# Performance work log

Measured on AMD Instinct MI355X. Metric: run time of the kernel, lower is better.

The kernel has to match this reference:

```python
import jax, jax.numpy as jnp
import numpy as np

D_MODEL = 512
N_HEADS = 8
D_FF = 2048

def _linear_params(key, d_in, d_out):
    kw, kb = jax.random.split(key)
    bound = 1.0 / np.sqrt(d_in)
    W = jax.random.uniform(kw, (d_in, d_out), minval=-bound, maxval=bound, dtype=jnp.float32)
    b = jax.random.uniform(kb, (d_out,), minval=-bound, maxval=bound, dtype=jnp.float32)
    return W, b

def setup_inputs() -> dict:
    key = jax.random.key(0)
    ks = jax.random.split(key, 7)
    x = jax.random.normal(ks[0], (4, 2048, D_MODEL), dtype=jnp.float32)
    Wq, bq = _linear_params(ks[1], D_MODEL, D_MODEL)
    Wk, bk = _linear_params(ks[2], D_MODEL, D_MODEL)
    Wv, bv = _linear_params(ks[3], D_MODEL, D_MODEL)
    W1, b1 = _linear_params(ks[4], D_MODEL, D_FF)
    W2, b2 = _linear_params(ks[5], D_FF, D_MODEL)
    g1 = jnp.ones((D_MODEL,), jnp.float32); be1 = jnp.zeros((D_MODEL,), jnp.float32)
    g2 = jnp.ones((D_MODEL,), jnp.float32); be2 = jnp.zeros((D_MODEL,), jnp.float32)
    return {"x": x, "Wq": Wq, "bq": bq, "Wk": Wk, "bk": bk, "Wv": Wv, "bv": bv,
            "W1": W1, "b1": b1, "W2": W2, "b2": b2,
            "g1": g1, "be1": be1, "g2": g2, "be2": be2}

def _layernorm(x, g, b, eps=1e-5):
    mu = jnp.mean(x, axis=-1, keepdims=True)
    var = jnp.mean(jnp.square(x - mu), axis=-1, keepdims=True)
    return (x - mu) * jax.lax.rsqrt(var + eps) * g + b

def reference(x, Wq, bq, Wk, bk, Wv, bv, W1, b1, W2, b2, g1, be1, g2, be2):
    B, S, D = x.shape
    H = N_HEADS
    Dh = D // H
    residual = x
    xn = _layernorm(x, g1, be1)
    # [B,S,D] -> [B,H,S,Dh]
    q = (xn @ Wq + bq).reshape(B, S, H, Dh).transpose(0, 2, 1, 3)
    k = (xn @ Wk + bk).reshape(B, S, H, Dh).transpose(0, 2, 1, 3)
    v = (xn @ Wv + bv).reshape(B, S, H, Dh).transpose(0, 2, 1, 3)
    # sigmoid pointwise attention, scaled by sqrt(d_model) (not head dim)
    scores = jnp.einsum('bhsd,bhtd->bhst', q, k) / jnp.sqrt(jnp.float32(D))
    attn = jax.nn.sigmoid(scores)
    out = jnp.einsum('bhst,bhtd->bhsd', attn, v)
    out = out.transpose(0, 2, 1, 3).reshape(B, S, D)
    x = residual + out  # dropout=0 (eval)
    residual = x
    xn = _layernorm(x, g2, be2)
    ffn = jax.nn.relu(xn @ W1 + b1) @ W2 + b2
    return residual + ffn
```

## Files before the change

### kernel.cpp

```cpp
#include <hip/hip_runtime.h>
#include <hip/hip_bf16.h>
#include <math.h>

#define D_MODEL 512
#define N_HEADS 8
#define D_HEAD 64
#define D_FF 2048
#define SEQ 2048
#define BATCH 4
#define NTOK (BATCH * SEQ)
#define QSCALE 0.04419417382415922f
#define QSCALE_L2E (-QSCALE * 1.44269504089f)

typedef unsigned short ushort_t;
typedef __attribute__((ext_vector_type(8))) short short8;
typedef __attribute__((ext_vector_type(4))) float float4v;

static __device__ __forceinline__ ushort_t f2bf(float f) {
    union { float f; unsigned int i; } c; c.f = f;
    unsigned int i = c.i;
    unsigned int r = (i + 0x7FFFu + ((i >> 16) & 1u)) >> 16;
    return (ushort_t)r;
}

static __device__ __forceinline__ unsigned int pack2bf(float a, float b) {
    union { __hip_bfloat162 h; unsigned int u; } c;
    c.h = __float22bfloat162_rn(make_float2(a, b));
    return c.u;
}

static __device__ __forceinline__ float sig2(float x) {
    return __builtin_amdgcn_rcpf(1.0f + __builtin_amdgcn_exp2f(x));
}

__global__ __launch_bounds__(256) void k_prep_weights(const float* __restrict__ Wq,
                                                      const float* __restrict__ Wk,
                                                      const float* __restrict__ Wv,
                                                      const float* __restrict__ W1,
                                                      const float* __restrict__ W2,
                                                      ushort_t* __restrict__ Wqkvt,
                                                      ushort_t* __restrict__ W1t,
                                                      ushort_t* __restrict__ W2t) {
    int id = blockIdx.x * 256 + threadIdx.x;
    if (id < 3 * 262144) {
        int m = id >> 18, r = id & 262143;
        int k = r >> 9, n = r & 511;
        const float* src = (m == 0) ? Wq : ((m == 1) ? Wk : Wv);
        Wqkvt[((size_t)m * 512 + n) * 512 + k] = f2bf(src[r]);
        return;
    }
    int id2 = id - 3 * 262144;
    if (id2 < 1048576) {
        int k = id2 >> 11, n = id2 & 2047;
        W1t[(size_t)n * 512 + k] = f2bf(W1[id2]);
        return;
    }
    int id3 = id2 - 1048576;
    if (id3 < 1048576) {
        int k = id3 >> 9, n = id3 & 511;
        W2t[(size_t)n * 2048 + k] = f2bf(W2[id3]);
    }
}

__global__ __launch_bounds__(256) void k_layernorm(const float* __restrict__ X,
                                                   const float* __restrict__ g,
                                                   const float* __restrict__ be,
                                                   ushort_t* __restrict__ Out) {
    int row  = blockIdx.x * 4 + (threadIdx.x >> 6);
    int lane = threadIdx.x & 63;
    const float* x = X + (size_t)row * D_MODEL + lane * 8;
    float4 v0 = ((const float4*)x)[0];
    float4 v1 = ((const float4*)x)[1];
    float vals[8] = {v0.x, v0.y, v0.z, v0.w, v1.x, v1.y, v1.z, v1.w};
    float s = 0.f, sq = 0.f;
#pragma unroll
    for (int j = 0; j < 8; j++) { s += vals[j]; sq += vals[j] * vals[j]; }
#pragma unroll
    for (int off = 32; off; off >>= 1) { s += __shfl_xor(s, off); sq += __shfl_xor(sq, off); }
    float mu  = s * (1.0f / D_MODEL);
    float var = sq * (1.0f / D_MODEL) - mu * mu;
    float inv = rsqrtf(var + 1e-5f);
    const float* gp  = g  + lane * 8;
    const float* bp  = be + lane * 8;
    float4 g0 = ((const float4*)gp)[0], g1v = ((const float4*)gp)[1];
    float4 b0 = ((const float4*)bp)[0], b1v = ((const float4*)bp)[1];
    float gs[8] = {g0.x, g0.y, g0.z, g0.w, g1v.x, g1v.y, g1v.z, g1v.w};
    float bs[8] = {b0.x, b0.y, b0.z, b0.w, b1v.x, b1v.y, b1v.z, b1v.w};
    ushort_t o[8];
#pragma unroll
    for (int j = 0; j < 8; j++) o[j] = f2bf((vals[j] - mu) * inv * gs[j] + bs[j]);
    ushort_t* op = Out + (size_t)row * D_MODEL + lane * 8;
    *(uint4*)op = *(uint4*)o;
}


static __device__ __forceinline__ void stage_tile(const ushort_t* __restrict__ G, int K,
                                                  ushort_t* L, int nchunks, int koff,
                                                  int w, int l) {
#pragma unroll
    for (int n = w; n < nchunks; n += 4) {
        const ushort_t* g = G + (size_t)(n * 16 + (l >> 2)) * K + koff + (l & 3) * 8;
        __builtin_amdgcn_global_load_lds((const __attribute__((address_space(1))) void*)g,
                                         (__attribute__((address_space(3))) void*)(L + n * 512),
                                         16, 0, 0);
    }
}

template <int JW>
static __device__ __forceinline__ void gemm_core2(const ushort_t* __restrict__ A,
                                                  const ushort_t* __restrict__ Bt,
                                                  int K, int m0, int n0,
                                                  ushort_t* As, ushort_t* Bs,
                                                  float4v acc[4][JW]) {
    const int BBUF = JW * 1024;
    int t = threadIdx.x, w = t >> 6, l = t & 63, q = l >> 4, lm = l & 15;
    int mb = (w & 1) * 64, nb = (w >> 1) * (JW * 16);
    const ushort_t* Ab = A + (size_t)m0 * K;
    const ushort_t* Bb = Bt + (size_t)n0 * K;
    int T = K >> 5;

    stage_tile(Ab, K, As, 8, 0, w, l);
    stage_tile(Bb, K, Bs, 2 * JW, 0, w, l);
    __syncthreads();

    for (int kt = 0; kt < T; kt++) {
        int cur = kt & 1;
        if (kt + 1 < T) {
            stage_tile(Ab, K, As + (1 - cur) * 4096, 8, (kt + 1) * 32, w, l);
            stage_tile(Bb, K, Bs + (1 - cur) * BBUF, 2 * JW, (kt + 1) * 32, w, l);
        }
        const ushort_t* asb = As + cur * 4096;
        const ushort_t* bsb = Bs + cur * BBUF;
        short8 a[4], b[JW];
#pragma unroll
        for (int i = 0; i < 4; i++) a[i] = *(const short8*)&asb[(mb + 16 * i + lm) * 32 + q * 8];
#pragma unroll
        for (int j = 0; j < JW; j++) b[j] = *(const short8*)&bsb[(nb + 16 * j + lm) * 32 + q * 8];
#pragma unroll
        for (int i = 0; i < 4; i++)
#pragma unroll
            for (int j = 0; j < JW; j++)
                acc[i][j] = __builtin_amdgcn_mfma_f32_16x16x32_bf16(a[i], b[j], acc[i][j], 0, 0, 0);
        __syncthreads();
    }
}

__global__ __launch_bounds__(256) void k_gemm_qkv(const ushort_t* __restrict__ A,
                                                  const ushort_t* __restrict__ Bt,
                                                  const float* __restrict__ bq,
                                                  const float* __restrict__ bk,
                                                  const float* __restrict__ bv,
                                                  ushort_t* __restrict__ qb,
                                                  ushort_t* __restrict__ kb,
                                                  ushort_t* __restrict__ vt) {
    __shared__ __align__(16) ushort_t As[8192];
    __shared__ __align__(16) ushort_t Bs[8192];
    int m0 = blockIdx.x * 128, n0 = blockIdx.y * 128;
    float4v acc[4][4];
#pragma unroll
    for (int i = 0; i < 4; i++)
#pragma unroll
        for (int j = 0; j < 4; j++) acc[i][j] = (float4v){0.f, 0.f, 0.f, 0.f};
    gemm_core2<4>(A, Bt, D_MODEL, m0, n0, As, Bs, acc);

    int t = threadIdx.x, w = t >> 6, l = t & 63, q = l >> 4, lm = l & 15;
    int mb = (w & 1) * 64, nb = (w >> 1) * 64;
    int mat = n0 >> 9, c0 = n0 & 511;
    const float* bias = (mat == 0) ? bq : ((mat == 1) ? bk : bv);
#pragma unroll
    for (int j = 0; j < 4; j++) {
        int cl = c0 + nb + 16 * j + lm;
        int hh = cl >> 6, dh = cl & 63;
        float bvv = bias[cl];
#pragma unroll
        for (int i = 0; i < 4; i++) {
            int mr0 = m0 + mb + 16 * i + q * 4;
            int bb = mr0 >> 11, ss0 = mr0 & (SEQ - 1);
            if (mat == 2) {
                union { ushort_t s[4]; uint2 v; } pk;
#pragma unroll
                for (int r = 0; r < 4; r++) pk.s[r] = f2bf(acc[i][j][r] + bvv);
                *(uint2*)&vt[((size_t)(bb * N_HEADS + hh) * D_HEAD + dh) * SEQ + ss0] = pk.v;
            } else {
                ushort_t* dst = (mat == 0) ? qb : kb;
                float sc = (mat == 0) ? QSCALE_L2E : 1.0f;
#pragma unroll
                for (int r = 0; r < 4; r++)
                    dst[((size_t)(bb * N_HEADS + hh) * SEQ + ss0 + r) * D_HEAD + dh] =
                        f2bf((acc[i][j][r] + bvv) * sc);
            }
        }
    }
}

__global__ __launch_bounds__(256) void k_gemm_ffn1(const ushort_t* __restrict__ A,
                                                   const ushort_t* __restrict__ Bt,
                                                   const float* __restrict__ b1,
                                                   ushort_t* __restrict__ hb) {
    __shared__ __align__(16) ushort_t As[8192];
    __shared__ __align__(16) ushort_t Bs[8192];
    int m0 = blockIdx.x * 128, n0 = blockIdx.y * 128;
    float4v acc[4][4];
#pragma unroll
    for (int i = 0; i < 4; i++)
#pragma unroll
        for (int j = 0; j < 4; j++) acc[i][j] = (float4v){0.f, 0.f, 0.f, 0.f};
    gemm_core2<4>(A, Bt, D_MODEL, m0, n0, As, Bs, acc);

    int t = threadIdx.x, w = t >> 6, l = t & 63, q = l >> 4, lm = l & 15;
    int mb = (w & 1) * 64, nb = (w >> 1) * 64;
#pragma unroll
    for (int j = 0; j < 4; j++) {
        int cl = n0 + nb + 16 * j + lm;
        float bvv = b1[cl];
#pragma unroll
        for (int i = 0; i < 4; i++) {
            int mr0 = m0 + mb + 16 * i + q * 4;
#pragma unroll
            for (int r = 0; r < 4; r++)
                hb[(size_t)(mr0 + r) * D_FF + cl] = f2bf(fmaxf(acc[i][j][r] + bvv, 0.f));
        }
    }
}

__global__ __launch_bounds__(256) void k_gemm_ffn2(const ushort_t* __restrict__ A,
                                                   const ushort_t* __restrict__ Bt,
                                                   const float* __restrict__ b2,
                                                   const float* __restrict__ res,
                                                   float* __restrict__ out) {
    __shared__ __align__(16) ushort_t As[8192];
    __shared__ __align__(16) ushort_t Bs[4096];
    int m0 = blockIdx.x * 128, n0 = blockIdx.y * 64;
    float4v acc[4][2];
#pragma unroll
    for (int i = 0; i < 4; i++)
#pragma unroll
        for (int j = 0; j < 2; j++) acc[i][j] = (float4v){0.f, 0.f, 0.f, 0.f};
    gemm_core2<2>(A, Bt, D_FF, m0, n0, As, Bs, acc);

    int t = threadIdx.x, w = t >> 6, l = t & 63, q = l >> 4, lm = l & 15;
    int mb = (w & 1) * 64, nb = (w >> 1) * 32;
#pragma unroll
    for (int j = 0; j < 2; j++) {
        int cl = n0 + nb + 16 * j + lm;
        float bvv = b2[cl];
#pragma unroll
        for (int i = 0; i < 4; i++) {
            int mr0 = m0 + mb + 16 * i + q * 4;
#pragma unroll
            for (int r = 0; r < 4; r++) {
                size_t idx = (size_t)(mr0 + r) * D_MODEL + cl;
                out[idx] = acc[i][j][r] + bvv + res[idx];
            }
        }
    }
}

__global__ __launch_bounds__(256) void k_attention(const ushort_t* __restrict__ Q,
                                                   const ushort_t* __restrict__ Kb,
                                                   const ushort_t* __restrict__ Vt,
                                                   const float* __restrict__ X,
                                                   float* __restrict__ Y) {
    __shared__ ushort_t Ks[2][64][72];
    __shared__ ushort_t Vs[2][64][72];
    __shared__ ushort_t Ps[128][72];
    int bh = blockIdx.y;
    int b = bh >> 3, h = bh & 7;
    size_t base = (size_t)bh * SEQ * D_HEAD;
    int s0 = blockIdx.x * 128;
    int t = threadIdx.x, w = t >> 6, l = t & 63, q = l >> 4, lm = l & 15;
    int srow = t >> 2, sc = (t & 3) * 16;

    short8 qf[2][2];
#pragma unroll
    for (int nt = 0; nt < 2; nt++)
#pragma unroll
        for (int kc = 0; kc < 2; kc++) {
            const ushort_t* qg = Q + base + (size_t)(s0 + 32 * w + 16 * nt + lm) * D_HEAD + kc * 32 + q * 8;
            uint4 u = *(const uint4*)qg;
            qf[nt][kc] = *(const short8*)&u;
        }

    float4v o[2][4];
#pragma unroll
    for (int nt = 0; nt < 2; nt++)
#pragma unroll
        for (int dj = 0; dj < 4; dj++) o[nt][dj] = (float4v){0.f, 0.f, 0.f, 0.f};

    uint4 kr0, kr1, vr0, vr1;
    const ushort_t* kg0 = Kb + base + (size_t)srow * D_HEAD + sc;
    const ushort_t* vg0 = Vt + base + (size_t)srow * SEQ + sc;

    kr0 = *(const uint4*)(kg0); kr1 = *(const uint4*)(kg0 + 8);
    vr0 = *(const uint4*)(vg0); vr1 = *(const uint4*)(vg0 + 8);
    *(uint4*)&Ks[0][srow][sc] = kr0; *(uint4*)&Ks[0][srow][sc + 8] = kr1;
    *(uint4*)&Vs[0][srow][sc] = vr0; *(uint4*)&Vs[0][srow][sc + 8] = vr1;
    kr0 = *(const uint4*)(kg0 + 64 * D_HEAD); kr1 = *(const uint4*)(kg0 + 64 * D_HEAD + 8);
    vr0 = *(const uint4*)(vg0 + 64);          vr1 = *(const uint4*)(vg0 + 64 + 8);
    __syncthreads();

    for (int tt = 0; tt < SEQ / 64; tt++) {
        int cur = tt & 1;
        float4v st[4][2];
#pragma unroll
        for (int mt = 0; mt < 4; mt++)
#pragma unroll
            for (int nt = 0; nt < 2; nt++) st[mt][nt] = (float4v){0.f, 0.f, 0.f, 0.f};
#pragma unroll
        for (int kc = 0; kc < 2; kc++) {
            short8 a[4];
#pragma unroll
            for (int mt = 0; mt < 4; mt++) a[mt] = *(const short8*)&Ks[cur][16 * mt + lm][kc * 32 + q * 8];
#pragma unroll
            for (int mt = 0; mt < 4; mt++)
#pragma unroll
                for (int nt = 0; nt < 2; nt++)
                    st[mt][nt] = __builtin_amdgcn_mfma_f32_16x16x32_bf16(a[mt], qf[nt][kc], st[mt][nt], 0, 0, 0);
        }
#pragma unroll
        for (int mt = 0; mt < 4; mt++)
#pragma unroll
            for (int nt = 0; nt < 2; nt++) {
                float4v s4 = st[mt][nt];
                uint2 pk;
                pk.x = pack2bf(sig2(s4[0]), sig2(s4[1]));
                pk.y = pack2bf(sig2(s4[2]), sig2(s4[3]));
                *(uint2*)&Ps[32 * w + 16 * nt + lm][16 * mt + 4 * q] = pk;
            }
#pragma unroll
        for (int kc = 0; kc < 2; kc++) {
            short8 ap[2], bv[4];
#pragma unroll
            for (int nt = 0; nt < 2; nt++) ap[nt] = *(const short8*)&Ps[32 * w + 16 * nt + lm][kc * 32 + q * 8];
#pragma unroll
            for (int dj = 0; dj < 4; dj++) bv[dj] = *(const short8*)&Vs[cur][16 * dj + lm][kc * 32 + q * 8];
#pragma unroll
            for (int nt = 0; nt < 2; nt++)
#pragma unroll
                for (int dj = 0; dj < 4; dj++)
                    o[nt][dj] = __builtin_amdgcn_mfma_f32_16x16x32_bf16(ap[nt], bv[dj], o[nt][dj], 0, 0, 0);
        }
        if (tt + 1 < SEQ / 64) {
            int nxt = 1 - cur;
            *(uint4*)&Ks[nxt][srow][sc] = kr0; *(uint4*)&Ks[nxt][srow][sc + 8] = kr1;
            *(uint4*)&Vs[nxt][srow][sc] = vr0; *(uint4*)&Vs[nxt][srow][sc + 8] = vr1;
            if (tt + 2 < SEQ / 64) {
                const ushort_t* kg = kg0 + (size_t)(tt + 2) * 64 * D_HEAD;
                const ushort_t* vg = vg0 + (tt + 2) * 64;
                kr0 = *(const uint4*)(kg); kr1 = *(const uint4*)(kg + 8);
                vr0 = *(const uint4*)(vg); vr1 = *(const uint4*)(vg + 8);
            }
        }
        __syncthreads();
    }

#pragma unroll
    for (int nt = 0; nt < 2; nt++)
#pragma unroll
        for (int dj = 0; dj < 4; dj++) {
            int d = 16 * dj + lm;
#pragma unroll
            for (int r = 0; r < 4; r++) {
                int s = s0 + 32 * w + 16 * nt + q * 4 + r;
                size_t idx = ((size_t)(b * SEQ + s)) * D_MODEL + h * D_HEAD + d;
                Y[idx] = X[idx] + o[nt][dj][r];
            }
        }
}

extern "C" void kernel_launch(void* const* d_in, const int* in_sizes, int n_in,
                              void* d_out, int out_size, void* d_ws, size_t ws_size,
                              hipStream_t stream) {
    const float* x   = (const float*)d_in[0];
    const float* Wq  = (const float*)d_in[1];
    const float* bq  = (const float*)d_in[2];
    const float* Wk  = (const float*)d_in[3];
    const float* bk  = (const float*)d_in[4];
    const float* Wv  = (const float*)d_in[5];
    const float* bv  = (const float*)d_in[6];
    const float* W1  = (const float*)d_in[7];
    const float* b1  = (const float*)d_in[8];
    const float* W2  = (const float*)d_in[9];
    const float* b2  = (const float*)d_in[10];
    const float* g1  = (const float*)d_in[11];
    const float* be1 = (const float*)d_in[12];
    const float* g2  = (const float*)d_in[13];
    const float* be2 = (const float*)d_in[14];
    float* out = (float*)d_out;

    char* p = (char*)d_ws;
    ushort_t* xn    = (ushort_t*)p; p += (size_t)NTOK * D_MODEL * 2;
    ushort_t* yn    = (ushort_t*)p; p += (size_t)NTOK * D_MODEL * 2;
    float*    y     = (float*)p;    p += (size_t)NTOK * D_MODEL * 4;
    ushort_t* qb    = (ushort_t*)p; p += (size_t)NTOK * D_MODEL * 2;
    ushort_t* kb    = (ushort_t*)p; p += (size_t)NTOK * D_MODEL * 2;
    ushort_t* vt    = (ushort_t*)p; p += (size_t)NTOK * D_MODEL * 2;
    ushort_t* hb    = (ushort_t*)p; p += (size_t)NTOK * D_FF * 2;
    ushort_t* Wqkvt = (ushort_t*)p; p += (size_t)3 * D_MODEL * D_MODEL * 2;
    ushort_t* W1t   = (ushort_t*)p; p += (size_t)D_MODEL * D_FF * 2;
    ushort_t* W2t   = (ushort_t*)p; p += (size_t)D_FF * D_MODEL * 2;

    k_prep_weights<<<(3 * 262144 + 2 * 1048576 + 255) / 256, 256, 0, stream>>>(
        Wq, Wk, Wv, W1, W2, Wqkvt, W1t, W2t);

    k_layernorm<<<NTOK / 4, 256, 0, stream>>>(x, g1, be1, xn);

    dim3 gq(NTOK / 128, (3 * D_MODEL) / 128);
    k_gemm_qkv<<<gq, 256, 0, stream>>>(xn, Wqkvt, bq, bk, bv, qb, kb, vt);

    dim3 ga(SEQ / 128, BATCH * N_HEADS);
    k_attention<<<ga, 256, 0, stream>>>(qb, kb, vt, x, y);

    k_layernorm<<<NTOK / 4, 256, 0, stream>>>(y, g2, be2, yn);

    dim3 g1d(NTOK / 128, D_FF / 128);
    k_gemm_ffn1<<<g1d, 256, 0, stream>>>(yn, W1t, b1, hb);
    dim3 g2d(NTOK / 128, D_MODEL / 64);
    k_gemm_ffn2<<<g2d, 256, 0, stream>>>(hb, W2t, b2, y, out);
}
```

Baseline: 263.0 us.

## Split attention key tiles across wave pairs and tile the weight transpose

The attention kernel now runs 512 threads. Two waves share each 32-query group and each handles half of every 64-key tile. The two partial outputs are summed through shared memory, and the residual add is written with vectorized float4 stores. Weight preparation becomes a 64x64 shared-memory tiled transpose, so global reads and writes are coalesced instead of strided. The goal is more waves per attention block to hide latency, at the cost of more shared memory, an extra reduction step and extra barriers.

```diff
diff --git a/kernel.cpp b/kernel.cpp
--- a/kernel.cpp
+++ b/kernel.cpp
@@ -41,24 +41,30 @@
                                                       ushort_t* __restrict__ Wqkvt,
                                                       ushort_t* __restrict__ W1t,
                                                       ushort_t* __restrict__ W2t) {
-    int id = blockIdx.x * 256 + threadIdx.x;
-    if (id < 3 * 262144) {
-        int m = id >> 18, r = id & 262143;
-        int k = r >> 9, n = r & 511;
-        const float* src = (m == 0) ? Wq : ((m == 1) ? Wk : Wv);
-        Wqkvt[((size_t)m * 512 + n) * 512 + k] = f2bf(src[r]);
-        return;
-    }
-    int id2 = id - 3 * 262144;
-    if (id2 < 1048576) {
-        int k = id2 >> 11, n = id2 & 2047;
-        W1t[(size_t)n * 512 + k] = f2bf(W1[id2]);
-        return;
-    }
-    int id3 = id2 - 1048576;
-    if (id3 < 1048576) {
-        int k = id3 >> 9, n = id3 & 511;
-        W2t[(size_t)n * 2048 + k] = f2bf(W2[id3]);
+    __shared__ ushort_t tile[64][66];
+    int bid = blockIdx.x;
+    const float* src; ushort_t* dst; int K, N, tk, tn;
+    if (bid < 192) {
+        int m = bid >> 6, r = bid & 63;
+        src = (m == 0) ? Wq : ((m == 1) ? Wk : Wv);
+        dst = Wqkvt + (size_t)m * 512 * 512; K = 512; N = 512; tk = r >> 3; tn = r & 7;
+    } else if (bid < 448) {
+        int r = bid - 192; src = W1; dst = W1t; K = 512; N = 2048; tk = r >> 5; tn = r & 31;
+    } else {
+        int r = bid - 448; src = W2; dst = W2t; K = 2048; N = 512; tk = r >> 3; tn = r & 7;
+    }
+    int k0 = tk * 64, n0 = tn * 64;
+    int rr = threadIdx.x >> 6, c = threadIdx.x & 63;
+#pragma unroll
+    for (int i = 0; i < 16; i++) {
+        int row = i * 4 + rr;
+        tile[row][c] = f2bf(src[(size_t)(k0 + row) * N + n0 + c]);
+    }
+    __syncthreads();
+#pragma unroll
+    for (int i = 0; i < 16; i++) {
+        int row = i * 4 + rr;
+        dst[(size_t)(n0 + row) * K + k0 + c] = tile[c][row];
     }
 }
 
@@ -92,7 +98,6 @@
     ushort_t* op = Out + (size_t)row * D_MODEL + lane * 8;
     *(uint4*)op = *(uint4*)o;
 }
-
 
 static __device__ __forceinline__ void stage_tile(const ushort_t* __restrict__ G, int K,
                                                   ushort_t* L, int nchunks, int koff,
@@ -256,27 +261,32 @@
     }
 }
 
-__global__ __launch_bounds__(256) void k_attention(const ushort_t* __restrict__ Q,
+__global__ __launch_bounds__(512) void k_attention(const ushort_t* __restrict__ Q,
                                                    const ushort_t* __restrict__ Kb,
                                                    const ushort_t* __restrict__ Vt,
                                                    const float* __restrict__ X,
                                                    float* __restrict__ Y) {
-    __shared__ ushort_t Ks[2][64][72];
-    __shared__ ushort_t Vs[2][64][72];
-    __shared__ ushort_t Ps[128][72];
+    __shared__ __align__(16) char smem[57344];
+    ushort_t* Ks = (ushort_t*)smem;
+    ushort_t* Vs = (ushort_t*)(smem + 18432);
+    ushort_t* Ps = (ushort_t*)(smem + 36864);
+    float*  Osum = (float*)smem;
+
     int bh = blockIdx.y;
     int b = bh >> 3, h = bh & 7;
     size_t base = (size_t)bh * SEQ * D_HEAD;
     int s0 = blockIdx.x * 128;
     int t = threadIdx.x, w = t >> 6, l = t & 63, q = l >> 4, lm = l & 15;
-    int srow = t >> 2, sc = (t & 3) * 16;
+    int g = w >> 1, th = w & 1;
+    int srow = t >> 3, sc = (t & 7) * 8;
+    ushort_t* Pw = Ps + w * 1280;
 
     short8 qf[2][2];
 #pragma unroll
     for (int nt = 0; nt < 2; nt++)
 #pragma unroll
         for (int kc = 0; kc < 2; kc++) {
-            const ushort_t* qg = Q + base + (size_t)(s0 + 32 * w + 16 * nt + lm) * D_HEAD + kc * 32 + q * 8;
+            const ushort_t* qg = Q + base + (size_t)(s0 + 32 * g + 16 * nt + lm) * D_HEAD + kc * 32 + q * 8;
             uint4 u = *(const uint4*)qg;
             qf[nt][kc] = *(const short8*)&u;
         }
@@ -287,85 +297,107 @@
 #pragma unroll
         for (int dj = 0; dj < 4; dj++) o[nt][dj] = (float4v){0.f, 0.f, 0.f, 0.f};
 
-    uint4 kr0, kr1, vr0, vr1;
+    uint4 kr, vr;
     const ushort_t* kg0 = Kb + base + (size_t)srow * D_HEAD + sc;
     const ushort_t* vg0 = Vt + base + (size_t)srow * SEQ + sc;
 
-    kr0 = *(const uint4*)(kg0); kr1 = *(const uint4*)(kg0 + 8);
-    vr0 = *(const uint4*)(vg0); vr1 = *(const uint4*)(vg0 + 8);
-    *(uint4*)&Ks[0][srow][sc] = kr0; *(uint4*)&Ks[0][srow][sc + 8] = kr1;
-    *(uint4*)&Vs[0][srow][sc] = vr0; *(uint4*)&Vs[0][srow][sc + 8] = vr1;
-    kr0 = *(const uint4*)(kg0 + 64 * D_HEAD); kr1 = *(const uint4*)(kg0 + 64 * D_HEAD + 8);
-    vr0 = *(const uint4*)(vg0 + 64);          vr1 = *(const uint4*)(vg0 + 64 + 8);
+    kr = *(const uint4*)(kg0); vr = *(const uint4*)(vg0);
+    *(uint4*)&Ks[srow * 72 + sc] = kr; *(uint4*)&Vs[srow * 72 + sc] = vr;
+    kr = *(const uint4*)(kg0 + 64 * D_HEAD); vr = *(const uint4*)(vg0 + 64);
     __syncthreads();
 
     for (int tt = 0; tt < SEQ / 64; tt++) {
         int cur = tt & 1;
-        float4v st[4][2];
-#pragma unroll
-        for (int mt = 0; mt < 4; mt++)
+        const ushort_t* ksb = Ks + cur * 4608;
+        const ushort_t* vsb = Vs + cur * 4608;
+        short8 kf[2][2];
+#pragma unroll
+        for (int mt = 0; mt < 2; mt++)
+#pragma unroll
+            for (int kc = 0; kc < 2; kc++)
+                kf[mt][kc] = *(const short8*)&ksb[(32 * th + 16 * mt + lm) * 72 + kc * 32 + q * 8];
+        short8 vf[4];
+#pragma unroll
+        for (int dj = 0; dj < 4; dj++)
+            vf[dj] = *(const short8*)&vsb[(16 * dj + lm) * 72 + th * 32 + q * 8];
+        float4v st[2][2];
+#pragma unroll
+        for (int mt = 0; mt < 2; mt++)
 #pragma unroll
             for (int nt = 0; nt < 2; nt++) st[mt][nt] = (float4v){0.f, 0.f, 0.f, 0.f};
 #pragma unroll
-        for (int kc = 0; kc < 2; kc++) {
-            short8 a[4];
-#pragma unroll
-            for (int mt = 0; mt < 4; mt++) a[mt] = *(const short8*)&Ks[cur][16 * mt + lm][kc * 32 + q * 8];
-#pragma unroll
-            for (int mt = 0; mt < 4; mt++)
+        for (int kc = 0; kc < 2; kc++)
+#pragma unroll
+            for (int mt = 0; mt < 2; mt++)
 #pragma unroll
                 for (int nt = 0; nt < 2; nt++)
-                    st[mt][nt] = __builtin_amdgcn_mfma_f32_16x16x32_bf16(a[mt], qf[nt][kc], st[mt][nt], 0, 0, 0);
-        }
-#pragma unroll
-        for (int mt = 0; mt < 4; mt++)
+                    st[mt][nt] = __builtin_amdgcn_mfma_f32_16x16x32_bf16(kf[mt][kc], qf[nt][kc], st[mt][nt], 0, 0, 0);
+#pragma unroll
+        for (int mt = 0; mt < 2; mt++)
 #pragma unroll
             for (int nt = 0; nt < 2; nt++) {
-                float4v s4 = st[mt][nt];
                 uint2 pk;
-                pk.x = pack2bf(sig2(s4[0]), sig2(s4[1]));
-                pk.y = pack2bf(sig2(s4[2]), sig2(s4[3]));
-                *(uint2*)&Ps[32 * w + 16 * nt + lm][16 * mt + 4 * q] = pk;
+                pk.x = pack2bf(sig2(st[mt][nt][0]), sig2(st[mt][nt][1]));
+                pk.y = pack2bf(sig2(st[mt][nt][2]), sig2(st[mt][nt][3]));
+                *(uint2*)&Pw[(16 * nt + lm) * 40 + 16 * mt + 4 * q] = pk;
             }
 #pragma unroll
-        for (int kc = 0; kc < 2; kc++) {
-            short8 ap[2], bv[4];
-#pragma unroll
-            for (int nt = 0; nt < 2; nt++) ap[nt] = *(const short8*)&Ps[32 * w + 16 * nt + lm][kc * 32 + q * 8];
-#pragma unroll
-            for (int dj = 0; dj < 4; dj++) bv[dj] = *(const short8*)&Vs[cur][16 * dj + lm][kc * 32 + q * 8];
-#pragma unroll
-            for (int nt = 0; nt < 2; nt++)
-#pragma unroll
-                for (int dj = 0; dj < 4; dj++)
-                    o[nt][dj] = __builtin_amdgcn_mfma_f32_16x16x32_bf16(ap[nt], bv[dj], o[nt][dj], 0, 0, 0);
+        for (int nt = 0; nt < 2; nt++) {
+            short8 ap = *(const short8*)&Pw[(16 * nt + lm) * 40 + q * 8];
+#pragma unroll
+            for (int dj = 0; dj < 4; dj++)
+                o[nt][dj] = __builtin_amdgcn_mfma_f32_16x16x32_bf16(ap, vf[dj], o[nt][dj], 0, 0, 0);
         }
         if (tt + 1 < SEQ / 64) {
             int nxt = 1 - cur;
-            *(uint4*)&Ks[nxt][srow][sc] = kr0; *(uint4*)&Ks[nxt][srow][sc + 8] = kr1;
-            *(uint4*)&Vs[nxt][srow][sc] = vr0; *(uint4*)&Vs[nxt][srow][sc + 8] = vr1;
+            *(uint4*)&Ks[nxt * 4608 + srow * 72 + sc] = kr;
+            *(uint4*)&Vs[nxt * 4608 + srow * 72 + sc] = vr;
             if (tt + 2 < SEQ / 64) {
-                const ushort_t* kg = kg0 + (size_t)(tt + 2) * 64 * D_HEAD;
-                const ushort_t* vg = vg0 + (tt + 2) * 64;
-                kr0 = *(const uint4*)(kg); kr1 = *(const uint4*)(kg + 8);
-                vr0 = *(const uint4*)(vg); vr1 = *(const uint4*)(vg + 8);
+                kr = *(const uint4*)(kg0 + (size_t)(tt + 2) * 64 * D_HEAD);
+                vr = *(const uint4*)(vg0 + (tt + 2) * 64);
             }
         }
         __syncthreads();
     }
 
-#pragma unroll
-    for (int nt = 0; nt < 2; nt++)
-#pragma unroll
-        for (int dj = 0; dj < 4; dj++) {
-            int d = 16 * dj + lm;
-#pragma unroll
-            for (int r = 0; r < 4; r++) {
-                int s = s0 + 32 * w + 16 * nt + q * 4 + r;
-                size_t idx = ((size_t)(b * SEQ + s)) * D_MODEL + h * D_HEAD + d;
-                Y[idx] = X[idx] + o[nt][dj][r];
-            }
-        }
+    __syncthreads();
+    if (th == 0) {
+#pragma unroll
+        for (int nt = 0; nt < 2; nt++)
+#pragma unroll
+            for (int dj = 0; dj < 4; dj++)
+#pragma unroll
+                for (int r = 0; r < 4; r++)
+                    Osum[(32 * g + 16 * nt + 4 * q + r) * 66 + 16 * dj + lm] = o[nt][dj][r];
+    }
+    __syncthreads();
+    if (th == 1) {
+#pragma unroll
+        for (int nt = 0; nt < 2; nt++)
+#pragma unroll
+            for (int dj = 0; dj < 4; dj++)
+#pragma unroll
+                for (int r = 0; r < 4; r++)
+                    Osum[(32 * g + 16 * nt + 4 * q + r) * 66 + 16 * dj + lm] += o[nt][dj][r];
+    }
+    __syncthreads();
+
+    {
+        int row = t >> 2, c0 = (t & 3) * 16;
+        size_t gro = ((size_t)(b * SEQ + s0 + row)) * D_MODEL + h * D_HEAD + c0;
+        const float* xp = X + gro;
+        float* yp = Y + gro;
+        const float* os = &Osum[row * 66 + c0];
+#pragma unroll
+        for (int i = 0; i < 4; i++) {
+            float4 xv = *(const float4*)(xp + i * 4);
+            float4 ov = *(const float4*)(os + i * 4);
+            float4 rr;
+            rr.x = xv.x + ov.x; rr.y = xv.y + ov.y;
+            rr.z = xv.z + ov.z; rr.w = xv.w + ov.w;
+            *(float4*)(yp + i * 4) = rr;
+        }
+    }
 }
 
 extern "C" void kernel_launch(void* const* d_in, const int* in_sizes, int n_in,
@@ -400,8 +432,7 @@
     ushort_t* W1t   = (ushort_t*)p; p += (size_t)D_MODEL * D_FF * 2;
     ushort_t* W2t   = (ushort_t*)p; p += (size_t)D_FF * D_MODEL * 2;
 
-    k_prep_weights<<<(3 * 262144 + 2 * 1048576 + 255) / 256, 256, 0, stream>>>(
-        Wq, Wk, Wv, W1, W2, Wqkvt, W1t, W2t);
+    k_prep_weights<<<704, 256, 0, stream>>>(Wq, Wk, Wv, W1, W2, Wqkvt, W1t, W2t);
 
     k_layernorm<<<NTOK / 4, 256, 0, stream>>>(x, g1, be1, xn);
 
@@ -409,7 +440,7 @@
     k_gemm_qkv<<<gq, 256, 0, stream>>>(xn, Wqkvt, bq, bk, bv, qb, kb, vt);
 
     dim3 ga(SEQ / 128, BATCH * N_HEADS);
-    k_attention<<<ga, 256, 0, stream>>>(qb, kb, vt, x, y);
+    k_attention<<<ga, 512, 0, stream>>>(qb, kb, vt, x, y);
 
     k_layernorm<<<NTOK / 4, 256, 0, stream>>>(y, g2, be2, yn);
 
```

Measured after the change: 245.1 us. 1.07x faster.
